# Kernel tuning notes

Measured on AMD Instinct MI355X. Metric: run time of the kernel, lower is better.

## Reference

```python
import jax, jax.numpy as jnp
import numpy as np

DEFOCUS_MAX = 4.0
R_MAX = int(DEFOCUS_MAX) + 1   # matches kernel's intRadius = int(fltRadius) + 1 at max defocus
GAMMA = 4.0                    # tanh sharpness of the soft disk edge
PI = 3.141592653589793


def setup_inputs():
    key = jax.random.key(0)
    k1, k2 = jax.random.split(key)
    B, C, H, W = 2, 3, 512, 512
    image = jax.random.uniform(k1, (B, C, H, W), dtype=jnp.float32)
    # signed per-pixel circle-of-confusion radius, scaled to [0, DEFOCUS_MAX)
    defocus = jax.random.uniform(k2, (B, 1, H, W), dtype=jnp.float32) * DEFOCUS_MAX
    return {"image": image, "defocus": defocus}


def _render(image, defocus):
    # Scatter form (CUDA kernel): every source pixel p splats w(p, dist) * image[p]
    # into all q with |q-p|_inf <= int(|defocus[p]|)+1, plus w into weight_cum.
    # Equivalent gather form used here: out[q] = sum over offsets o of
    # w(q-o, |o|) * image[q-o], vectorized over all pixels per offset.
    B, C, H, W = image.shape
    R = R_MAX
    r = jnp.abs(defocus)                              # CoC radius per source pixel
    int_r = jnp.floor(r) + 1.0                        # square scatter window half-size
    inv_area = 1.0 / jnp.maximum(PI * r * r, 1.0)     # disk-area normalization

    pad = ((0, 0), (0, 0), (R, R), (R, R))
    img_p = jnp.pad(image, pad)
    r_p = jnp.pad(r, pad)
    ir_p = jnp.pad(int_r, pad)
    inv_p = jnp.pad(inv_area, pad)
    val_p = jnp.pad(jnp.ones((B, 1, H, W), jnp.float32), pad)  # in-bounds source mask

    offs = np.stack(np.meshgrid(np.arange(-R, R + 1), np.arange(-R, R + 1),
                                indexing='ij'), -1).reshape(-1, 2)
    offs = jnp.asarray(offs, jnp.int32)               # ((2R+1)^2, 2)

    def body(carry, off):
        bokeh, wsum = carry
        dy, dx = off[0], off[1]
        y0, x0 = R - dy, R - dx                       # source p = q - (dy, dx)
        src_img = jax.lax.dynamic_slice(img_p, (0, 0, y0, x0), (B, C, H, W))
        src_r = jax.lax.dynamic_slice(r_p, (0, 0, y0, x0), (B, 1, H, W))
        src_ir = jax.lax.dynamic_slice(ir_p, (0, 0, y0, x0), (B, 1, H, W))
        src_inv = jax.lax.dynamic_slice(inv_p, (0, 0, y0, x0), (B, 1, H, W))
        src_val = jax.lax.dynamic_slice(val_p, (0, 0, y0, x0), (B, 1, H, W))
        dist = jnp.sqrt((dy * dy + dx * dx).astype(jnp.float32))
        in_win = (jnp.abs(dy).astype(jnp.float32) <= src_ir) & \
                 (jnp.abs(dx).astype(jnp.float32) <= src_ir)
        w = (0.5 + 0.5 * jnp.tanh(GAMMA * (src_r - dist))) * src_inv
        w = jnp.where(in_win, w, 0.0) * src_val
        return (bokeh + w * src_img, wsum + w), None

    init = (jnp.zeros((B, C, H, W), jnp.float32),
            jnp.zeros((B, 1, H, W), jnp.float32))
    (bokeh_cum, weight_cum), _ = jax.lax.scan(jax.checkpoint(body), init, offs)
    return bokeh_cum / weight_cum


def reference(image, defocus):
    return _render(image, defocus)
```

## Files before the change

kernel.cpp:

```cpp
#include <hip/hip_runtime.h>
#include <cmath>


#define HH 512
#define WW 512
#define NB 2
#define TW 64
#define TH 16
#define HALO 4
#define SROWS (TH + 2 * HALO)
#define LW 72

typedef float v2f __attribute__((ext_vector_type(2)));

__device__ __forceinline__ unsigned rtne_hi(float v) {
  unsigned u = __float_as_uint(v);
  u = u + 0x7FFFu + ((u >> 16) & 1u);
  return u & 0xFFFF0000u;
}

__global__ __launch_bounds__(512, 4) void bokeh_gather(
    const float* __restrict__ img,
    const float* __restrict__ def,
    float* __restrict__ out)
{
  __shared__ __align__(16) unsigned sX[SROWS][LW];
  __shared__ __align__(16) unsigned sY[SROWS][LW];
  __shared__ __align__(16) unsigned sZ[SROWS][LW];
  __shared__ float sFd[9][12];
  __shared__ __align__(16) float pbuf[256][20];

  const int tid = threadIdx.x;
  const int s   = tid >> 8;
  const int t   = tid & 255;
  const int tx  = t & 15;
  const int ty  = t >> 4;
  const int bx = blockIdx.x * TW;
  const int by = blockIdx.y * TH;
  const int b  = blockIdx.z;

  if (tid < 81) {
    int dyi = tid / 9, dxi = tid - dyi * 9;
    int dyo = dyi - 4, dxo = dxi - 4;
    float d2 = (float)(dyo * dyo + dxo * dxo);
    sFd[dyi][dxi] = __expf(8.0f * sqrtf(d2));
  }

  const float* dpt = def + b * (HH * WW);
  const float* ipt = img + b * (3 * HH * WW);

  for (int idx = tid; idx < SROWS * LW; idx += 512) {
    int ly = idx / LW;
    int lx = idx - ly * LW;
    int sy = by - HALO + ly;
    int sx = bx - HALO + lx;
    unsigned X, Y = 0u, Z = 0u;
    if ((unsigned)sy < (unsigned)HH && (unsigned)sx < (unsigned)WW) {
      int o = sy * WW + sx;
      float r = fabsf(dpt[o]);
      float J  = fmaxf(3.14159265358979f * r * r, 1.0f);
      float Hv = __expf(-8.0f * r) * J;
      X = rtne_hi(J) | (rtne_hi(Hv) >> 16);
      Y = rtne_hi(ipt[o]) | (rtne_hi(ipt[o + HH * WW]) >> 16);
      Z = __float_as_uint(ipt[o + 2 * HH * WW]) & 0xFFFF0000u;
    } else {
      X = rtne_hi(1e30f);
    }
    sX[ly][lx] = X;
    sY[ly][lx] = Y;
    sZ[ly][lx] = Z;
  }
  __syncthreads();

  v2f a01[4] = {{0.f,0.f},{0.f,0.f},{0.f,0.f},{0.f,0.f}};
  v2f a2w[4] = {{0.f,0.f},{0.f,0.f},{0.f,0.f},{0.f,0.f}};

  const int col0 = 4 * tx;
  const int dy0 = s ? 5 : 0;
  const int dy1 = s ? 9 : 5;

  #pragma unroll 1
  for (int dy = dy0; dy < dy1; ++dy) {
    const int sr = ty + dy;
    float fdr[9];
    #pragma unroll
    for (int x = 0; x < 9; ++x) fdr[x] = sFd[dy][x];

    unsigned Xv[12], Yv[12], Zv[12];
    #pragma unroll
    for (int q = 0; q < 3; ++q) {
      *(uint4*)&Xv[4 * q] = *(const uint4*)(&sX[sr][col0] + 4 * q);
      *(uint4*)&Yv[4 * q] = *(const uint4*)(&sY[sr][col0] + 4 * q);
      *(uint4*)&Zv[4 * q] = *(const uint4*)(&sZ[sr][col0] + 4 * q);
    }
    float Jv[12], Hv[12];
    v2f C01[12], Z1[12];
    #pragma unroll
    for (int j = 0; j < 12; ++j) {
      Jv[j] = __uint_as_float(Xv[j] & 0xFFFF0000u);
      Hv[j] = __uint_as_float(Xv[j] << 16);
      C01[j] = (v2f){__uint_as_float(Yv[j] & 0xFFFF0000u),
                     __uint_as_float(Yv[j] << 16)};
      Z1[j]  = (v2f){__uint_as_float(Zv[j]), 1.0f};
    }

    #pragma unroll
    for (int k = 0; k < 4; ++k) {
      #pragma unroll
      for (int j = k; j < k + 9; ++j) {
        const int xi = j - k;
        float tden = fmaf(Hv[j], fdr[xi], Jv[j]);
        float w = __builtin_amdgcn_rcpf(tden);
        v2f wp = (v2f){w, w};
        a01[k] = __builtin_elementwise_fma(wp, C01[j], a01[k]);
        a2w[k] = __builtin_elementwise_fma(wp, Z1[j],  a2w[k]);
      }
    }
  }

  if (s == 1) {
    *(float4*)&pbuf[t][0]  = make_float4(a2w[0].y, a2w[1].y, a2w[2].y, a2w[3].y);
    *(float4*)&pbuf[t][4]  = make_float4(a01[0].x, a01[1].x, a01[2].x, a01[3].x);
    *(float4*)&pbuf[t][8]  = make_float4(a01[0].y, a01[1].y, a01[2].y, a01[3].y);
    *(float4*)&pbuf[t][12] = make_float4(a2w[0].x, a2w[1].x, a2w[2].x, a2w[3].x);
  }
  __syncthreads();
  if (s == 0) {
    float4 v0 = *(const float4*)&pbuf[t][0];
    float4 v1 = *(const float4*)&pbuf[t][4];
    float4 v2 = *(const float4*)&pbuf[t][8];
    float4 v3 = *(const float4*)&pbuf[t][12];
    float wsum[4] = {a2w[0].y + v0.x, a2w[1].y + v0.y,
                     a2w[2].y + v0.z, a2w[3].y + v0.w};
    float ac0[4]  = {a01[0].x + v1.x, a01[1].x + v1.y,
                     a01[2].x + v1.z, a01[3].x + v1.w};
    float ac1[4]  = {a01[0].y + v2.x, a01[1].y + v2.y,
                     a01[2].y + v2.z, a01[3].y + v2.w};
    float ac2[4]  = {a2w[0].x + v3.x, a2w[1].x + v3.y,
                     a2w[2].x + v3.z, a2w[3].x + v3.w};

    const int oy = by + ty;
    const int ox = bx + col0;
    float rw[4];
    #pragma unroll
    for (int k = 0; k < 4; ++k) rw[k] = __builtin_amdgcn_rcpf(wsum[k]);

    float* op0 = out + ((b * 3 + 0) * HH + oy) * WW + ox;
    float* op1 = out + ((b * 3 + 1) * HH + oy) * WW + ox;
    float* op2 = out + ((b * 3 + 2) * HH + oy) * WW + ox;
    float4 o0, o1, o2;
    o0.x = ac0[0] * rw[0]; o0.y = ac0[1] * rw[1]; o0.z = ac0[2] * rw[2]; o0.w = ac0[3] * rw[3];
    o1.x = ac1[0] * rw[0]; o1.y = ac1[1] * rw[1]; o1.z = ac1[2] * rw[2]; o1.w = ac1[3] * rw[3];
    o2.x = ac2[0] * rw[0]; o2.y = ac2[1] * rw[1]; o2.z = ac2[2] * rw[2]; o2.w = ac2[3] * rw[3];
    *(float4*)op0 = o0;
    *(float4*)op1 = o1;
    *(float4*)op2 = o2;
  }
}

extern "C" void kernel_launch(void* const* d_in, const int* in_sizes, int n_in,
                              void* d_out, int out_size, void* d_ws, size_t ws_size,
                              hipStream_t stream) {
  const float* img = (const float*)d_in[0];
  const float* def = (const float*)d_in[1];
  float* out = (float*)d_out;

  dim3 grid(WW / TW, HH / TH, NB);
  dim3 block(512);
  hipLaunchKernelGGL(bokeh_gather, grid, block, 0, stream, img, def, out);
}
```

Baseline: 16.85 us.

## Process both batches per block with register prefetch and trim far corner taps

Each block now handles both batch images instead of one, which halves the grid. The second batch's defocus and image values are loaded into registers while the first batch is computed, then packed into a second shared-memory buffer, so global load latency overlaps with the first tile's math. Separately, the outermost tap rows (|dy|=3,4) skip the far-corner dx taps, whose distance exceeds the maximum radius and whose weights are tiny. The changes trade grid-level parallelism and extra shared memory and registers for overlapped loads and fewer taps, and the tap trimming slightly changes the numerics.

```diff
diff --git a/kernel.cpp b/kernel.cpp
--- a/kernel.cpp
+++ b/kernel.cpp
@@ -4,12 +4,12 @@
 
 #define HH 512
 #define WW 512
-#define NB 2
 #define TW 64
 #define TH 16
 #define HALO 4
 #define SROWS (TH + 2 * HALO)
 #define LW 72
+#define NENT (SROWS * LW)
 
 typedef float v2f __attribute__((ext_vector_type(2)));
 
@@ -17,6 +17,27 @@
   unsigned u = __float_as_uint(v);
   u = u + 0x7FFFu + ((u >> 16) & 1u);
   return u & 0xFFFF0000u;
+}
+
+template <int XLO, int XHI>
+__device__ __forceinline__ void tap_rows(const float* __restrict__ fdr,
+                                         const float* __restrict__ Jv,
+                                         const float* __restrict__ Hv,
+                                         const v2f* __restrict__ C01,
+                                         const v2f* __restrict__ Z1,
+                                         v2f (&a01)[4], v2f (&a2w)[4]) {
+  #pragma unroll
+  for (int k = 0; k < 4; ++k) {
+    #pragma unroll
+    for (int xi = XLO; xi < XHI; ++xi) {
+      const int j = k + xi;
+      float tden = fmaf(Hv[j], fdr[xi], Jv[j]);
+      float w = __builtin_amdgcn_rcpf(tden);
+      v2f wp = {w, w};
+      a01[k] = __builtin_elementwise_fma(wp, C01[j], a01[k]);
+      a2w[k] = __builtin_elementwise_fma(wp, Z1[j], a2w[k]);
+    }
+  }
 }
 
 __global__ __launch_bounds__(512, 4) void bokeh_gather(
@@ -24,9 +45,9 @@
     const float* __restrict__ def,
     float* __restrict__ out)
 {
-  __shared__ __align__(16) unsigned sX[SROWS][LW];
-  __shared__ __align__(16) unsigned sY[SROWS][LW];
-  __shared__ __align__(16) unsigned sZ[SROWS][LW];
+  __shared__ __align__(16) unsigned sX[2][SROWS][LW];
+  __shared__ __align__(16) unsigned sY[2][SROWS][LW];
+  __shared__ __align__(16) unsigned sZ[2][SROWS][LW];
   __shared__ float sFd[9][12];
   __shared__ __align__(16) float pbuf[256][20];
 
@@ -37,7 +58,6 @@
   const int ty  = t >> 4;
   const int bx = blockIdx.x * TW;
   const int by = blockIdx.y * TH;
-  const int b  = blockIdx.z;
 
   if (tid < 81) {
     int dyi = tid / 9, dxi = tid - dyi * 9;
@@ -46,116 +66,164 @@
     sFd[dyi][dxi] = __expf(8.0f * sqrtf(d2));
   }
 
-  const float* dpt = def + b * (HH * WW);
-  const float* ipt = img + b * (3 * HH * WW);
-
-  for (int idx = tid; idx < SROWS * LW; idx += 512) {
-    int ly = idx / LW;
-    int lx = idx - ly * LW;
-    int sy = by - HALO + ly;
-    int sx = bx - HALO + lx;
-    unsigned X, Y = 0u, Z = 0u;
-    if ((unsigned)sy < (unsigned)HH && (unsigned)sx < (unsigned)WW) {
+  {
+    const float* dpt = def;
+    const float* ipt = img;
+    for (int idx = tid; idx < NENT; idx += 512) {
+      int ly = idx / LW;
+      int lx = idx - ly * LW;
+      int sy = by - HALO + ly;
+      int sx = bx - HALO + lx;
+      unsigned X, Y = 0u, Z = 0u;
+      if ((unsigned)sy < (unsigned)HH && (unsigned)sx < (unsigned)WW) {
+        int o = sy * WW + sx;
+        float r = fabsf(dpt[o]);
+        float J  = fmaxf(3.14159265358979f * r * r, 1.0f);
+        float Hv = __expf(-8.0f * r) * J;
+        X = rtne_hi(J) | (rtne_hi(Hv) >> 16);
+        Y = rtne_hi(ipt[o]) | (rtne_hi(ipt[o + HH * WW]) >> 16);
+        Z = __float_as_uint(ipt[o + 2 * HH * WW]) & 0xFFFF0000u;
+      } else {
+        X = rtne_hi(1e30f);
+      }
+      sX[0][ly][lx] = X;
+      sY[0][ly][lx] = Y;
+      sZ[0][ly][lx] = Z;
+    }
+  }
+  __syncthreads();
+
+  float r1v[4], c0v[4], c1v[4], c2v[4];
+  {
+    const float* dpt = def + HH * WW;
+    const float* ipt = img + 3 * HH * WW;
+    #pragma unroll
+    for (int i = 0; i < 4; ++i) {
+      int idx = tid + 512 * i;
+      int ly = idx / LW;
+      int lx = idx - ly * LW;
+      int sy = by - HALO + ly;
+      int sx = bx - HALO + lx;
+      bool inb = (idx < NENT) &&
+                 (unsigned)sy < (unsigned)HH && (unsigned)sx < (unsigned)WW;
       int o = sy * WW + sx;
-      float r = fabsf(dpt[o]);
-      float J  = fmaxf(3.14159265358979f * r * r, 1.0f);
-      float Hv = __expf(-8.0f * r) * J;
-      X = rtne_hi(J) | (rtne_hi(Hv) >> 16);
-      Y = rtne_hi(ipt[o]) | (rtne_hi(ipt[o + HH * WW]) >> 16);
-      Z = __float_as_uint(ipt[o + 2 * HH * WW]) & 0xFFFF0000u;
-    } else {
-      X = rtne_hi(1e30f);
-    }
-    sX[ly][lx] = X;
-    sY[ly][lx] = Y;
-    sZ[ly][lx] = Z;
-  }
-  __syncthreads();
-
-  v2f a01[4] = {{0.f,0.f},{0.f,0.f},{0.f,0.f},{0.f,0.f}};
-  v2f a2w[4] = {{0.f,0.f},{0.f,0.f},{0.f,0.f},{0.f,0.f}};
+      r1v[i] = inb ? dpt[o] : -1.0f;
+      c0v[i] = inb ? ipt[o] : 0.0f;
+      c1v[i] = inb ? ipt[o + HH * WW] : 0.0f;
+      c2v[i] = inb ? ipt[o + 2 * HH * WW] : 0.0f;
+    }
+  }
 
   const int col0 = 4 * tx;
   const int dy0 = s ? 5 : 0;
   const int dy1 = s ? 9 : 5;
 
-  #pragma unroll 1
-  for (int dy = dy0; dy < dy1; ++dy) {
-    const int sr = ty + dy;
-    float fdr[9];
-    #pragma unroll
-    for (int x = 0; x < 9; ++x) fdr[x] = sFd[dy][x];
-
-    unsigned Xv[12], Yv[12], Zv[12];
-    #pragma unroll
-    for (int q = 0; q < 3; ++q) {
-      *(uint4*)&Xv[4 * q] = *(const uint4*)(&sX[sr][col0] + 4 * q);
-      *(uint4*)&Yv[4 * q] = *(const uint4*)(&sY[sr][col0] + 4 * q);
-      *(uint4*)&Zv[4 * q] = *(const uint4*)(&sZ[sr][col0] + 4 * q);
-    }
-    float Jv[12], Hv[12];
-    v2f C01[12], Z1[12];
-    #pragma unroll
-    for (int j = 0; j < 12; ++j) {
-      Jv[j] = __uint_as_float(Xv[j] & 0xFFFF0000u);
-      Hv[j] = __uint_as_float(Xv[j] << 16);
-      C01[j] = (v2f){__uint_as_float(Yv[j] & 0xFFFF0000u),
-                     __uint_as_float(Yv[j] << 16)};
-      Z1[j]  = (v2f){__uint_as_float(Zv[j]), 1.0f};
-    }
-
-    #pragma unroll
-    for (int k = 0; k < 4; ++k) {
-      #pragma unroll
-      for (int j = k; j < k + 9; ++j) {
-        const int xi = j - k;
-        float tden = fmaf(Hv[j], fdr[xi], Jv[j]);
-        float w = __builtin_amdgcn_rcpf(tden);
-        v2f wp = (v2f){w, w};
-        a01[k] = __builtin_elementwise_fma(wp, C01[j], a01[k]);
-        a2w[k] = __builtin_elementwise_fma(wp, Z1[j],  a2w[k]);
-      }
-    }
-  }
-
-  if (s == 1) {
-    *(float4*)&pbuf[t][0]  = make_float4(a2w[0].y, a2w[1].y, a2w[2].y, a2w[3].y);
-    *(float4*)&pbuf[t][4]  = make_float4(a01[0].x, a01[1].x, a01[2].x, a01[3].x);
-    *(float4*)&pbuf[t][8]  = make_float4(a01[0].y, a01[1].y, a01[2].y, a01[3].y);
-    *(float4*)&pbuf[t][12] = make_float4(a2w[0].x, a2w[1].x, a2w[2].x, a2w[3].x);
-  }
+  auto compute_tile = [&](int q, v2f (&a01)[4], v2f (&a2w)[4]) {
+    #pragma unroll 1
+    for (int dy = dy0; dy < dy1; ++dy) {
+      const int sr = ty + dy;
+      float fdr[9];
+      #pragma unroll
+      for (int x = 0; x < 9; ++x) fdr[x] = sFd[dy][x];
+
+      unsigned Xv[12], Yv[12], Zv[12];
+      #pragma unroll
+      for (int qq = 0; qq < 3; ++qq) {
+        *(uint4*)&Xv[4 * qq] = *(const uint4*)(&sX[q][sr][col0] + 4 * qq);
+        *(uint4*)&Yv[4 * qq] = *(const uint4*)(&sY[q][sr][col0] + 4 * qq);
+        *(uint4*)&Zv[4 * qq] = *(const uint4*)(&sZ[q][sr][col0] + 4 * qq);
+      }
+      float Jv[12], Hv[12];
+      v2f C01[12], Z1[12];
+      #pragma unroll
+      for (int j = 0; j < 12; ++j) {
+        Jv[j] = __uint_as_float(Xv[j] & 0xFFFF0000u);
+        Hv[j] = __uint_as_float(Xv[j] << 16);
+        C01[j] = (v2f){__uint_as_float(Yv[j] & 0xFFFF0000u),
+                       __uint_as_float(Yv[j] << 16)};
+        Z1[j]  = (v2f){__uint_as_float(Zv[j]), 1.0f};
+      }
+
+      const int ady = dy < 4 ? 4 - dy : dy - 4;
+      if (ady == 4)      tap_rows<2, 7>(fdr, Jv, Hv, C01, Z1, a01, a2w);
+      else if (ady == 3) tap_rows<1, 8>(fdr, Jv, Hv, C01, Z1, a01, a2w);
+      else               tap_rows<0, 9>(fdr, Jv, Hv, C01, Z1, a01, a2w);
+    }
+  };
+
+  auto combine_write = [&](int b, v2f (&a01)[4], v2f (&a2w)[4]) {
+    if (s == 1) {
+      *(float4*)&pbuf[t][0]  = make_float4(a2w[0].y, a2w[1].y, a2w[2].y, a2w[3].y);
+      *(float4*)&pbuf[t][4]  = make_float4(a01[0].x, a01[1].x, a01[2].x, a01[3].x);
+      *(float4*)&pbuf[t][8]  = make_float4(a01[0].y, a01[1].y, a01[2].y, a01[3].y);
+      *(float4*)&pbuf[t][12] = make_float4(a2w[0].x, a2w[1].x, a2w[2].x, a2w[3].x);
+    }
+    __syncthreads();
+    if (s == 0) {
+      float4 v0 = *(const float4*)&pbuf[t][0];
+      float4 v1 = *(const float4*)&pbuf[t][4];
+      float4 v2 = *(const float4*)&pbuf[t][8];
+      float4 v3 = *(const float4*)&pbuf[t][12];
+      float wsum[4] = {a2w[0].y + v0.x, a2w[1].y + v0.y,
+                       a2w[2].y + v0.z, a2w[3].y + v0.w};
+      float ac0[4]  = {a01[0].x + v1.x, a01[1].x + v1.y,
+                       a01[2].x + v1.z, a01[3].x + v1.w};
+      float ac1[4]  = {a01[0].y + v2.x, a01[1].y + v2.y,
+                       a01[2].y + v2.z, a01[3].y + v2.w};
+      float ac2[4]  = {a2w[0].x + v3.x, a2w[1].x + v3.y,
+                       a2w[2].x + v3.z, a2w[3].x + v3.w};
+      const int oy = by + ty;
+      const int ox = bx + col0;
+      float rw[4];
+      #pragma unroll
+      for (int k = 0; k < 4; ++k) rw[k] = __builtin_amdgcn_rcpf(wsum[k]);
+      float* op0 = out + ((b * 3 + 0) * HH + oy) * WW + ox;
+      float* op1 = out + ((b * 3 + 1) * HH + oy) * WW + ox;
+      float* op2 = out + ((b * 3 + 2) * HH + oy) * WW + ox;
+      float4 o0, o1, o2;
+      o0.x = ac0[0]*rw[0]; o0.y = ac0[1]*rw[1]; o0.z = ac0[2]*rw[2]; o0.w = ac0[3]*rw[3];
+      o1.x = ac1[0]*rw[0]; o1.y = ac1[1]*rw[1]; o1.z = ac1[2]*rw[2]; o1.w = ac1[3]*rw[3];
+      o2.x = ac2[0]*rw[0]; o2.y = ac2[1]*rw[1]; o2.z = ac2[2]*rw[2]; o2.w = ac2[3]*rw[3];
+      *(float4*)op0 = o0;
+      *(float4*)op1 = o1;
+      *(float4*)op2 = o2;
+    }
+  };
+
+  v2f a01[4] = {{0.f,0.f},{0.f,0.f},{0.f,0.f},{0.f,0.f}};
+  v2f a2w[4] = {{0.f,0.f},{0.f,0.f},{0.f,0.f},{0.f,0.f}};
+  compute_tile(0, a01, a2w);
+
+  #pragma unroll
+  for (int i = 0; i < 4; ++i) {
+    int idx = tid + 512 * i;
+    if (idx < NENT) {
+      int ly = idx / LW;
+      int lx = idx - ly * LW;
+      unsigned X, Y = 0u, Z = 0u;
+      if (r1v[i] >= 0.0f) {
+        float r = r1v[i];
+        float J  = fmaxf(3.14159265358979f * r * r, 1.0f);
+        float Hv = __expf(-8.0f * r) * J;
+        X = rtne_hi(J) | (rtne_hi(Hv) >> 16);
+        Y = rtne_hi(c0v[i]) | (rtne_hi(c1v[i]) >> 16);
+        Z = __float_as_uint(c2v[i]) & 0xFFFF0000u;
+      } else {
+        X = rtne_hi(1e30f);
+      }
+      sX[1][ly][lx] = X;
+      sY[1][ly][lx] = Y;
+      sZ[1][ly][lx] = Z;
+    }
+  }
+
+  combine_write(0, a01, a2w);
   __syncthreads();
-  if (s == 0) {
-    float4 v0 = *(const float4*)&pbuf[t][0];
-    float4 v1 = *(const float4*)&pbuf[t][4];
-    float4 v2 = *(const float4*)&pbuf[t][8];
-    float4 v3 = *(const float4*)&pbuf[t][12];
-    float wsum[4] = {a2w[0].y + v0.x, a2w[1].y + v0.y,
-                     a2w[2].y + v0.z, a2w[3].y + v0.w};
-    float ac0[4]  = {a01[0].x + v1.x, a01[1].x + v1.y,
-                     a01[2].x + v1.z, a01[3].x + v1.w};
-    float ac1[4]  = {a01[0].y + v2.x, a01[1].y + v2.y,
-                     a01[2].y + v2.z, a01[3].y + v2.w};
-    float ac2[4]  = {a2w[0].x + v3.x, a2w[1].x + v3.y,
-                     a2w[2].x + v3.z, a2w[3].x + v3.w};
-
-    const int oy = by + ty;
-    const int ox = bx + col0;
-    float rw[4];
-    #pragma unroll
-    for (int k = 0; k < 4; ++k) rw[k] = __builtin_amdgcn_rcpf(wsum[k]);
-
-    float* op0 = out + ((b * 3 + 0) * HH + oy) * WW + ox;
-    float* op1 = out + ((b * 3 + 1) * HH + oy) * WW + ox;
-    float* op2 = out + ((b * 3 + 2) * HH + oy) * WW + ox;
-    float4 o0, o1, o2;
-    o0.x = ac0[0] * rw[0]; o0.y = ac0[1] * rw[1]; o0.z = ac0[2] * rw[2]; o0.w = ac0[3] * rw[3];
-    o1.x = ac1[0] * rw[0]; o1.y = ac1[1] * rw[1]; o1.z = ac1[2] * rw[2]; o1.w = ac1[3] * rw[3];
-    o2.x = ac2[0] * rw[0]; o2.y = ac2[1] * rw[1]; o2.z = ac2[2] * rw[2]; o2.w = ac2[3] * rw[3];
-    *(float4*)op0 = o0;
-    *(float4*)op1 = o1;
-    *(float4*)op2 = o2;
-  }
+
+  #pragma unroll
+  for (int k = 0; k < 4; ++k) { a01[k] = (v2f){0.f,0.f}; a2w[k] = (v2f){0.f,0.f}; }
+  compute_tile(1, a01, a2w);
+  combine_write(1, a01, a2w);
 }
 
 extern "C" void kernel_launch(void* const* d_in, const int* in_sizes, int n_in,
@@ -165,7 +233,7 @@
   const float* def = (const float*)d_in[1];
   float* out = (float*)d_out;
 
-  dim3 grid(WW / TW, HH / TH, NB);
+  dim3 grid(WW / TW, HH / TH, 1);
   dim3 block(512);
   hipLaunchKernelGGL(bokeh_gather, grid, block, 0, stream, img, def, out);
 }
```

New measurement: 36.95 us. 119% more time.
